# Optimization experiments

Measured on AMD Instinct MI355X. Metric: run time of the kernel, lower is better.

Reference implementation:

```python
import jax, jax.numpy as jnp
import numpy as np

N, E, B = 10000, 160000, 256
IN, DESC = 57, 1217
# (in_dim, heads, out_per_head) for the 4 GATConv layers
CONV_DIMS = [(57, 5, 114), (570, 5, 171), (855, 5, 114), (570, 1, 570)]
FC_DIMS = [(1024 + DESC, 1024), (1024, 2048), (2048, 1024), (1024, 256), (256, 1)]


def setup_inputs() -> dict:
    key = jax.random.key(0)
    cnt = [0]
    def p(shape, scale=0.05):
        cnt[0] += 1
        return jax.random.normal(jax.random.fold_in(key, cnt[0]), shape, jnp.float32) * scale
    d = {}
    d["x"] = jax.random.normal(jax.random.fold_in(key, 100), (N, IN), jnp.float32)
    d["edge_index"] = jax.random.randint(jax.random.fold_in(key, 101), (2, E), 0, N)
    d["batch"] = jnp.sort(jax.random.randint(jax.random.fold_in(key, 102), (N,), 0, B))
    d["desc"] = jax.random.normal(jax.random.fold_in(key, 103), (B, DESC), jnp.float32)
    for i, (ci, H, C) in enumerate(CONV_DIMS, 1):
        d[f"W{i}"] = p((ci, H * C))
        d[f"as{i}"] = p((H, C))
        d[f"ad{i}"] = p((H, C))
        d[f"b{i}"] = jnp.zeros((H * C,), jnp.float32)
    d["Wg"] = p((570, 1024)); d["bg"] = jnp.zeros((1024,), jnp.float32)
    for i, (ci, co) in enumerate(FC_DIMS, 1):
        d[f"Wf{i}"] = p((ci, co))
        d[f"bf{i}"] = jnp.zeros((co,), jnp.float32)
    return d


def gat_conv(x, src, dst, W, a_src, a_dst, b):
    """PyG GATConv (eval mode: attention dropout off), self-loops already in src/dst."""
    n = x.shape[0]
    H, C = a_src.shape
    h = (x @ W).reshape(n, H, C)                      # [N,H,C]
    al_s = (h * a_src).sum(-1)                         # [N,H]
    al_d = (h * a_dst).sum(-1)                         # [N,H]
    e = jax.nn.leaky_relu(al_s[src] + al_d[dst], 0.2)  # [E,H]
    # segment softmax over destination node
    m = jax.ops.segment_max(e, dst, num_segments=n)
    e = jnp.exp(e - m[dst])
    s = jax.ops.segment_sum(e, dst, num_segments=n)
    alpha = e / (s[dst] + 1e-16)                       # [E,H]
    msg = h[src] * alpha[:, :, None]                   # [E,H,C]
    out = jax.ops.segment_sum(msg, dst, num_segments=n)
    return out.reshape(n, H * C) + b


def reference(x, edge_index, batch, desc,
              W1, as1, ad1, b1, W2, as2, ad2, b2,
              W3, as3, ad3, b3, W4, as4, ad4, b4,
              Wg, bg, Wf1, bf1, Wf2, bf2, Wf3, bf3, Wf4, bf4, Wf5, bf5):
    n = x.shape[0]
    loops = jnp.arange(n)
    src = jnp.concatenate([edge_index[0], loops])
    dst = jnp.concatenate([edge_index[1], loops])
    h = x
    for W, a_s, a_d, b in [(W1, as1, ad1, b1), (W2, as2, ad2, b2),
                           (W3, as3, ad3, b3), (W4, as4, ad4, b4)]:
        h = jax.nn.relu(gat_conv(h, src, dst, W, a_s, a_d, b))
    pooled = jax.ops.segment_sum(h, batch, num_segments=B)   # global_add_pool [B,570]
    g = pooled @ Wg + bg
    z = jnp.concatenate([g, desc], axis=1)                    # [B, 2241]
    z = jax.nn.relu(z @ Wf1 + bf1)
    z = jax.nn.relu(z @ Wf2 + bf2)
    z = jax.nn.relu(z @ Wf3 + bf3)
    z = jax.nn.relu(z @ Wf4 + bf4)
    return z @ Wf5 + bf5                                      # [B,1]
```

## Files before the change

kernel.cpp:

```cpp
#include <hip/hip_runtime.h>
#include <hip/hip_bf16.h>
#include <math.h>

#define NNODES 10000
#define NEDGES 160000
#define NB     256
#define ETOT   (NEDGES + NNODES)
#define INDIM  57
#define DESCD  1217

static inline size_t align256(size_t x) { return (x + 255) & ~size_t(255); }

typedef _Float16 half8_t __attribute__((ext_vector_type(8)));
typedef _Float16 half4v_t __attribute__((ext_vector_type(4)));
typedef _Float16 half2_t __attribute__((ext_vector_type(2)));
typedef float f32x4 __attribute__((ext_vector_type(4)));

__device__ inline float wave_max(float v) {
#pragma unroll
  for (int o = 32; o > 0; o >>= 1) v = fmaxf(v, __shfl_xor(v, o));
  return v;
}
__device__ inline float wave_sum(float v) {
#pragma unroll
  for (int o = 32; o > 0; o >>= 1) v += __shfl_xor(v, o);
  return v;
}

__global__ void count_kernel(const int* __restrict__ ei, int* __restrict__ deg) {
  int e = blockIdx.x * blockDim.x + threadIdx.x;
  if (e < ETOT) {
    int dst = (e < NEDGES) ? ei[NEDGES + e] : (e - NEDGES);
    atomicAdd(&deg[dst], 1);
  }
}

__global__ __launch_bounds__(1024) void scan_kernel(const int* __restrict__ deg,
                                                    int* __restrict__ row_ptr,
                                                    int* __restrict__ cursor) {
  __shared__ int part[1024];
  const int CHUNK = (NNODES + 1023) / 1024;
  int t = threadIdx.x;
  int start = t * CHUNK;
  int sum = 0;
  for (int i = 0; i < CHUNK; ++i) {
    int idx = start + i;
    if (idx < NNODES) sum += deg[idx];
  }
  part[t] = sum;
  __syncthreads();
  for (int off = 1; off < 1024; off <<= 1) {
    int v = (t >= off) ? part[t - off] : 0;
    __syncthreads();
    part[t] += v;
    __syncthreads();
  }
  int run = (t > 0) ? part[t - 1] : 0;
  for (int i = 0; i < CHUNK; ++i) {
    int idx = start + i;
    if (idx < NNODES) {
      row_ptr[idx] = run;
      cursor[idx] = run;
      run += deg[idx];
    }
  }
  if (t == 1023) row_ptr[NNODES] = ETOT;
}

__global__ void scatter_kernel(const int* __restrict__ ei, int* __restrict__ cursor,
                               int* __restrict__ csr_src) {
  int e = blockIdx.x * blockDim.x + threadIdx.x;
  if (e < ETOT) {
    int src, dst;
    if (e < NEDGES) { src = ei[e]; dst = ei[NEDGES + e]; }
    else            { src = e - NEDGES; dst = src; }
    int idx = atomicAdd(&cursor[dst], 1);
    csr_src[idx] = src;
  }
}

__global__ void convert_x_kernel(const float* __restrict__ x, _Float16* __restrict__ x16) {
  int t = blockIdx.x * blockDim.x + threadIdx.x;
  if (t >= NNODES * 64) return;
  int n = t >> 6, k = t & 63;
  x16[t] = (_Float16)((k < INDIM) ? x[n * INDIM + k] : 0.f);
}

struct TMat { const float* src; _Float16* dst; int K, N, Kpad, tiles_k, tile_base;
              int Cn, Cnp, Ck, Ckp; };
struct TParams { TMat m[9]; };

__global__ __launch_bounds__(256) void transpose_w_kernel(TParams P, int nm) {
  __shared__ float tile[64][65];
  int bt = blockIdx.x;
  int mi = 0;
#pragma unroll
  for (int i = 1; i < 9; ++i)
    if (i < nm && bt >= P.m[i].tile_base) mi = i;
  TMat m = P.m[mi];
  int lt = bt - m.tile_base;
  int tk = lt % m.tiles_k, tn = lt / m.tiles_k;
  int k0 = tk * 64, n0 = tn * 64;
  int c = threadIdx.x & 63, r4 = threadIdx.x >> 6;
#pragma unroll
  for (int i = 0; i < 16; ++i) {
    int kr = r4 + i * 4;
    int gk = k0 + kr, gn = n0 + c;
    tile[kr][c] = (gk < m.K && gn < m.N) ? m.src[(size_t)gk * m.N + gn] : 0.f;
  }
  __syncthreads();
#pragma unroll
  for (int i = 0; i < 16; ++i) {
    int nr = r4 + i * 4;
    int gn = n0 + nr, gk = k0 + c;
    if (gn < m.N && gk < m.K) {
      int np = gn + (gn / m.Cn) * (m.Cnp - m.Cn);
      int kp = gk + (gk / m.Ck) * (m.Ckp - m.Ck);
      m.dst[(size_t)np * m.Kpad + kp] = (_Float16)tile[c][nr];
    }
  }
}

struct LMat { const float* W; const float* as; const float* ad; _Float16* dst;
              int K, HC, C, H, Kpad, la, wave_base, Ck, Ckp; };

__global__ __launch_bounds__(256) void logitw_kernel(LMat m0, LMat m1, LMat m2, LMat m3,
                                                     int nwaves) {
  int gw = (blockIdx.x * 256 + threadIdx.x) >> 6;
  int lane = threadIdx.x & 63;
  if (gw >= nwaves) return;
  LMat m = m3;
  if (gw < m1.wave_base) m = m0;
  else if (gw < m2.wave_base) m = m1;
  else if (gw < m3.wave_base) m = m2;
  int li = gw - m.wave_base;
  int H2 = 2 * m.H;
  int k = li / H2, r = li - k * H2;
  int h = (r >= m.H) ? r - m.H : r;
  const float* a = (r >= m.H) ? m.ad : m.as;
  float s = 0.f;
  for (int c = lane; c < m.C; c += 64)
    s += m.W[(size_t)k * m.HC + h * m.C + c] * a[h * m.C + c];
  s = wave_sum(s);
  int kp = k + (k / m.Ck) * (m.Ckp - m.Ck);
  if (lane == 0) m.dst[(size_t)(m.la + r) * m.Kpad + kp] = (_Float16)s;
}

__global__ void pooled16_kernel(const float* __restrict__ pooled, _Float16* __restrict__ p16) {
  int t = blockIdx.x * blockDim.x + threadIdx.x;
  if (t >= NB * 576) return;
  int b = t / 576, c = t - b * 576;
  p16[t] = (_Float16)((c < 570) ? pooled[b * 570 + c] : 0.f);
}

__global__ void desc_fill_kernel(const float* __restrict__ desc, _Float16* __restrict__ z16) {
  int t = blockIdx.x * blockDim.x + threadIdx.x;
  if (t >= NB * 1280) return;
  int b = t / 1280, i = t - b * 1280;
  z16[(size_t)b * 2304 + 1024 + i] = (_Float16)((i < DESCD) ? desc[b * DESCD + i] : 0.f);
}

__global__ __launch_bounds__(256) void mfma_gemm_kernel(
    const _Float16* __restrict__ A, const _Float16* __restrict__ Bt,
    _Float16* __restrict__ C, int M, int Kpad, int Nreal, int ldc) {
  __shared__ __align__(16) char smem[32768];
  char* AsB = smem;
  char* BsB = smem + 16384;
  int tid = threadIdx.x;
  int lane = tid & 63, wid = tid >> 6;
  int l15 = lane & 15, g = lane >> 4;
  int wr = wid >> 1, wc = wid & 1;
  int m0 = blockIdx.y * 128, n0 = blockIdx.x * 128;
  f32x4 acc[4][4];
#pragma unroll
  for (int i = 0; i < 4; ++i)
#pragma unroll
    for (int j = 0; j < 4; ++j) acc[i][j] = (f32x4){0.f, 0.f, 0.f, 0.f};

  int KT = Kpad >> 6;
  half8_t pa[4], pb[4];
#pragma unroll
  for (int i = 0; i < 4; ++i) {
    int r = i * 32 + (tid >> 3);
    int cs = (tid & 7) ^ (r & 7);
    int ga = min(m0 + r, M - 1);
    pa[i] = *(const half8_t*)(A + (size_t)ga * Kpad + cs * 8);
    pb[i] = *(const half8_t*)(Bt + (size_t)(n0 + r) * Kpad + cs * 8);
  }
  for (int kt = 0; kt < KT; ++kt) {
    __syncthreads();
#pragma unroll
    for (int i = 0; i < 4; ++i) {
      *(half8_t*)(AsB + i * 4096 + tid * 16) = pa[i];
      *(half8_t*)(BsB + i * 4096 + tid * 16) = pb[i];
    }
    __syncthreads();
    if (kt + 1 < KT) {
      int k0 = (kt + 1) << 6;
#pragma unroll
      for (int i = 0; i < 4; ++i) {
        int r = i * 32 + (tid >> 3);
        int cs = (tid & 7) ^ (r & 7);
        int ga = min(m0 + r, M - 1);
        pa[i] = *(const half8_t*)(A + (size_t)ga * Kpad + k0 + cs * 8);
        pb[i] = *(const half8_t*)(Bt + (size_t)(n0 + r) * Kpad + k0 + cs * 8);
      }
    }
#pragma unroll
    for (int kk = 0; kk < 2; ++kk) {
      half8_t af[4], bf[4];
#pragma unroll
      for (int f = 0; f < 4; ++f) {
        int ra = wr * 64 + f * 16 + l15;
        af[f] = *(const half8_t*)(AsB + ra * 128 + (((kk * 4 + g) ^ (ra & 7)) << 4));
        int cb = wc * 64 + f * 16 + l15;
        bf[f] = *(const half8_t*)(BsB + cb * 128 + (((kk * 4 + g) ^ (cb & 7)) << 4));
      }
#pragma unroll
      for (int fm = 0; fm < 4; ++fm)
#pragma unroll
        for (int fn = 0; fn < 4; ++fn)
          acc[fm][fn] = __builtin_amdgcn_mfma_f32_16x16x32_f16(af[fm], bf[fn], acc[fm][fn], 0, 0, 0);
    }
  }
#pragma unroll
  for (int fm = 0; fm < 4; ++fm) {
    int gmb = m0 + wr * 64 + fm * 16 + g * 4;
#pragma unroll
    for (int fn = 0; fn < 4; ++fn) {
      int gn = n0 + wc * 64 + fn * 16 + l15;
      if (gn >= Nreal) continue;
#pragma unroll
      for (int j = 0; j < 4; ++j) {
        int gm = gmb + j;
        if (gm < M) C[(size_t)gm * ldc + gn] = (_Float16)acc[fm][fn][j];
      }
    }
  }
}

__global__ __launch_bounds__(256) void mfma_splitk_kernel(
    const _Float16* __restrict__ A, const _Float16* __restrict__ Bt,
    float* __restrict__ P, int M, int Kpad, int N, int ktpc) {
  __shared__ __align__(16) char smem[32768];
  char* AsB = smem;
  char* BsB = smem + 16384;
  int tid = threadIdx.x;
  int lane = tid & 63, wid = tid >> 6;
  int l15 = lane & 15, g = lane >> 4;
  int wr = wid >> 1, wc = wid & 1;
  int m0 = blockIdx.y * 128, n0 = blockIdx.x * 128;
  int z = blockIdx.z;
  int KT = Kpad >> 6;
  int ktb = z * ktpc;
  int kte = min(KT, ktb + ktpc);
  f32x4 acc[4][4];
#pragma unroll
  for (int i = 0; i < 4; ++i)
#pragma unroll
    for (int j = 0; j < 4; ++j) acc[i][j] = (f32x4){0.f, 0.f, 0.f, 0.f};

  half8_t pa[4], pb[4];
  {
    int k0 = ktb << 6;
#pragma unroll
    for (int i = 0; i < 4; ++i) {
      int r = i * 32 + (tid >> 3);
      int cs = (tid & 7) ^ (r & 7);
      int ga = min(m0 + r, M - 1);
      pa[i] = *(const half8_t*)(A + (size_t)ga * Kpad + k0 + cs * 8);
      pb[i] = *(const half8_t*)(Bt + (size_t)(n0 + r) * Kpad + k0 + cs * 8);
    }
  }
  for (int kt = ktb; kt < kte; ++kt) {
    __syncthreads();
#pragma unroll
    for (int i = 0; i < 4; ++i) {
      *(half8_t*)(AsB + i * 4096 + tid * 16) = pa[i];
      *(half8_t*)(BsB + i * 4096 + tid * 16) = pb[i];
    }
    __syncthreads();
    if (kt + 1 < kte) {
      int k0 = (kt + 1) << 6;
#pragma unroll
      for (int i = 0; i < 4; ++i) {
        int r = i * 32 + (tid >> 3);
        int cs = (tid & 7) ^ (r & 7);
        int ga = min(m0 + r, M - 1);
        pa[i] = *(const half8_t*)(A + (size_t)ga * Kpad + k0 + cs * 8);
        pb[i] = *(const half8_t*)(Bt + (size_t)(n0 + r) * Kpad + k0 + cs * 8);
      }
    }
#pragma unroll
    for (int kk = 0; kk < 2; ++kk) {
      half8_t af[4], bf[4];
#pragma unroll
      for (int f = 0; f < 4; ++f) {
        int ra = wr * 64 + f * 16 + l15;
        af[f] = *(const half8_t*)(AsB + ra * 128 + (((kk * 4 + g) ^ (ra & 7)) << 4));
        int cb = wc * 64 + f * 16 + l15;
        bf[f] = *(const half8_t*)(BsB + cb * 128 + (((kk * 4 + g) ^ (cb & 7)) << 4));
      }
#pragma unroll
      for (int fm = 0; fm < 4; ++fm)
#pragma unroll
        for (int fn = 0; fn < 4; ++fn)
          acc[fm][fn] = __builtin_amdgcn_mfma_f32_16x16x32_f16(af[fm], bf[fn], acc[fm][fn], 0, 0, 0);
    }
  }
  size_t zb = (size_t)z * M;
#pragma unroll
  for (int fm = 0; fm < 4; ++fm) {
    int gmb = m0 + wr * 64 + fm * 16 + g * 4;
#pragma unroll
    for (int fn = 0; fn < 4; ++fn) {
      int gn = n0 + wc * 64 + fn * 16 + l15;
      if (gn >= N) continue;
#pragma unroll
      for (int j = 0; j < 4; ++j) {
        int gm = gmb + j;
        if (gm < M) P[(zb + gm) * N + gn] = acc[fm][fn][j];
      }
    }
  }
}

__global__ void reduce16_kernel(const float* __restrict__ P, const float* __restrict__ bias,
                                _Float16* __restrict__ O, int M, int N, int ldo,
                                int S, int relu) {
  int idx = blockIdx.x * blockDim.x + threadIdx.x;
  if (idx >= M * ldo) return;
  int row = idx / ldo, col = idx - row * ldo;
  if (col >= N) return;
  float s = bias[col];
  int MN = M * N;
  for (int z = 0; z < S; ++z) s += P[(size_t)z * MN + row * N + col];
  if (relu) s = fmaxf(s, 0.f);
  O[idx] = (_Float16)s;
}

__global__ __launch_bounds__(256) void fc5_kernel(const _Float16* __restrict__ A,
                                                  const float* __restrict__ w,
                                                  const float* __restrict__ b,
                                                  float* __restrict__ out) {
  int wid = threadIdx.x >> 6, lane = threadIdx.x & 63;
  int m = blockIdx.x * 4 + wid;
  if (m >= NB) return;
  float s = 0.f;
  for (int k = lane; k < 256; k += 64) s += (float)A[m * 256 + k] * w[k];
  s = wave_sum(s);
  if (lane == 0) out[m] = s + b[0];
}

template <int H>
__global__ __launch_bounds__(256) void att_kernel_t(const _Float16* __restrict__ hbuf,
                                                    int ldh, int la,
                                                    const int* __restrict__ row_ptr,
                                                    const int* __restrict__ csr_src,
                                                    _Float16* __restrict__ alpha_t,
                                                    half8_t* __restrict__ e8,
                                                    float* __restrict__ sinv) {
  int wid = threadIdx.x >> 6, lane = threadIdx.x & 63;
  int n = blockIdx.x * 4 + wid;
  if (n >= NNODES) return;
  int rp = row_ptr[n], deg = row_ptr[n + 1] - rp;
  float ad[H], m[H], ssum[H];
#pragma unroll
  for (int h = 0; h < H; ++h) {
    ad[h] = (float)hbuf[(size_t)n * ldh + la + H + h];
    m[h] = -1e30f; ssum[h] = 0.f;
  }
  for (int j = lane; j < deg; j += 64) {
    int s = csr_src[rp + j];
    half8_t v = *(const half8_t*)(hbuf + (size_t)s * ldh + la);
    half8_t ev{};
#pragma unroll
    for (int h = 0; h < H; ++h) {
      float e = (float)v[h] + ad[h];
      e = (e >= 0.f) ? e : 0.2f * e;
      ev[h] = (_Float16)e;
      m[h] = fmaxf(m[h], e);
    }
    e8[rp + j] = ev;
  }
#pragma unroll
  for (int h = 0; h < H; ++h) m[h] = wave_max(fmaxf(m[h], -1e30f));
  for (int j = lane; j < deg; j += 64) {
    half8_t ev = e8[rp + j];
#pragma unroll
    for (int h = 0; h < H; ++h) {
      float e = (float)ev[h] - m[h];
      e = (e > 0.f) ? 0.f : e;
      float x = expf(e);
      ssum[h] += x;
      alpha_t[(size_t)h * ETOT + rp + j] = (_Float16)x;
    }
  }
#pragma unroll
  for (int h = 0; h < H; ++h) {
    float s = wave_sum(ssum[h]);
    if (lane == 0) sinv[h * NNODES + n] = 1.f / (s + 1e-16f);
  }
}

__global__ __launch_bounds__(256) void agg_kernel(const _Float16* __restrict__ hbuf,
                                                  const _Float16* __restrict__ alpha_t,
                                                  const int* __restrict__ row_ptr,
                                                  const int* __restrict__ csr_src,
                                                  const float* __restrict__ bias,
                                                  const float* __restrict__ sinv,
                                                  _Float16* __restrict__ h16o,
                                                  int C, int Cpad, int ldh, int ldo,
                                                  int HCpad, int nchunks) {
  int wid = threadIdx.x >> 6, lane = threadIdx.x & 63;
  int gw = blockIdx.x * 4 + wid;
  int n = gw / nchunks, chunk = gw - n * nchunks;
  if (n >= NNODES) return;
  int k0 = chunk * 512 + lane * 8;
  if (k0 >= ldo) return;
  _Float16* op = h16o + (size_t)n * ldo + k0;
  if (k0 >= HCpad) { *(half8_t*)op = (half8_t){}; return; }
  int h0 = k0 / Cpad;
  int off = k0 - h0 * Cpad;
  const _Float16* A0 = alpha_t + (size_t)h0 * ETOT;
  const _Float16* hb = hbuf + k0;
  int rp = row_ptr[n], re = row_ptr[n + 1];
  half2_t acc0{}, acc1{}, acc2{}, acc3{};
  auto step = [&](int s, _Float16 a) {
    half8_t v = *(const half8_t*)(hb + (size_t)s * ldh);
    half2_t av{a, a};
    acc0 += av * half2_t{v[0], v[1]};
    acc1 += av * half2_t{v[2], v[3]};
    acc2 += av * half2_t{v[4], v[5]};
    acc3 += av * half2_t{v[6], v[7]};
  };
  int j = rp;
  for (; j < re && (j & 3); ++j) step(csr_src[j], A0[j]);
  for (; j + 8 <= re; j += 8) {
    int4 sa = *(const int4*)(csr_src + j);
    int4 sb = *(const int4*)(csr_src + j + 4);
    half4v_t aa = *(const half4v_t*)(A0 + j);
    half4v_t ab = *(const half4v_t*)(A0 + j + 4);
    step(sa.x, aa[0]); step(sa.y, aa[1]); step(sa.z, aa[2]); step(sa.w, aa[3]);
    step(sb.x, ab[0]); step(sb.y, ab[1]); step(sb.z, ab[2]); step(sb.w, ab[3]);
  }
  for (; j + 4 <= re; j += 4) {
    int4 sa = *(const int4*)(csr_src + j);
    half4v_t aa = *(const half4v_t*)(A0 + j);
    step(sa.x, aa[0]); step(sa.y, aa[1]); step(sa.z, aa[2]); step(sa.w, aa[3]);
  }
  for (; j < re; ++j) step(csr_src[j], A0[j]);
  float sc = sinv[h0 * NNODES + n];
  int base = h0 * C + off;
  int nreal = C - off;
  float af[8] = {(float)acc0[0], (float)acc0[1], (float)acc1[0], (float)acc1[1],
                 (float)acc2[0], (float)acc2[1], (float)acc3[0], (float)acc3[1]};
  half8_t o;
#pragma unroll
  for (int i = 0; i < 8; ++i) {
    float bv = bias[base + ((i < nreal) ? i : 0)];
    o[i] = (i < nreal) ? (_Float16)fmaxf(af[i] * sc + bv, 0.f) : (_Float16)0.f;
  }
  *(half8_t*)op = o;
}

__global__ __launch_bounds__(256) void pool_kernel(const _Float16* __restrict__ h4,
                                                   const int* __restrict__ batch,
                                                   float* __restrict__ pooled, int F, int ldh) {
  int wid = threadIdx.x >> 6, lane = threadIdx.x & 63;
  int n = blockIdx.x * 4 + wid;
  if (n >= NNODES) return;
  int b = batch[n];
  for (int k = lane; k < F; k += 64)
    atomicAdd(&pooled[(size_t)b * F + k], (float)h4[(size_t)n * ldh + k]);
}

extern "C" void kernel_launch(void* const* d_in, const int* in_sizes, int n_in,
                              void* d_out, int out_size, void* d_ws, size_t ws_size,
                              hipStream_t stream) {
  const float* x    = (const float*)d_in[0];
  const int*   ei   = (const int*)d_in[1];
  const int*   batch= (const int*)d_in[2];
  const float* desc = (const float*)d_in[3];
  const float* W1 = (const float*)d_in[4];  const float* as1 = (const float*)d_in[5];
  const float* ad1 = (const float*)d_in[6]; const float* b1 = (const float*)d_in[7];
  const float* W2 = (const float*)d_in[8];  const float* as2 = (const float*)d_in[9];
  const float* ad2 = (const float*)d_in[10];const float* b2 = (const float*)d_in[11];
  const float* W3 = (const float*)d_in[12]; const float* as3 = (const float*)d_in[13];
  const float* ad3 = (const float*)d_in[14];const float* b3 = (const float*)d_in[15];
  const float* W4 = (const float*)d_in[16]; const float* as4 = (const float*)d_in[17];
  const float* ad4 = (const float*)d_in[18];const float* b4 = (const float*)d_in[19];
  const float* Wg = (const float*)d_in[20]; const float* bg = (const float*)d_in[21];
  const float* Wf1 = (const float*)d_in[22];const float* bf1 = (const float*)d_in[23];
  const float* Wf2 = (const float*)d_in[24];const float* bf2 = (const float*)d_in[25];
  const float* Wf3 = (const float*)d_in[26];const float* bf3 = (const float*)d_in[27];
  const float* Wf4 = (const float*)d_in[28];const float* bf4 = (const float*)d_in[29];
  const float* Wf5 = (const float*)d_in[30];const float* bf5 = (const float*)d_in[31];
  float* out = (float*)d_out;

  char* p = (char*)d_ws;
  size_t off = 0;
  auto alloc = [&](size_t bytes) -> char* {
    char* r = p + off;
    off = align256(off + bytes);
    return r;
  };
  int*      deg     = (int*)alloc(sizeof(int) * NNODES);
  int*      row_ptr = (int*)alloc(sizeof(int) * (NNODES + 1));
  int*      cursor  = (int*)alloc(sizeof(int) * NNODES);
  int*      csr_src = (int*)alloc(sizeof(int) * ETOT);
  _Float16* alpha_t = (_Float16*)alloc(sizeof(_Float16) * (size_t)5 * ETOT);
  half8_t*  e8      = (half8_t*)alloc(sizeof(half8_t) * (size_t)ETOT);
  float*    sinv    = (float*)alloc(sizeof(float) * 5 * NNODES);
  _Float16* x16     = (_Float16*)alloc(sizeof(_Float16) * (size_t)NNODES * 64);
  _Float16* hA16    = (_Float16*)alloc(sizeof(_Float16) * ((size_t)NNODES * 896 + 1024));
  _Float16* h16     = (_Float16*)alloc(sizeof(_Float16) * ((size_t)NNODES * 896 + 1024));
  size_t wt_begin = off;
  _Float16* WtL1 = (_Float16*)alloc(sizeof(_Float16) * 640 * 64);
  _Float16* WtL2 = (_Float16*)alloc(sizeof(_Float16) * 896 * 640);
  _Float16* WtL3 = (_Float16*)alloc(sizeof(_Float16) * 640 * 896);
  _Float16* WtL4 = (_Float16*)alloc(sizeof(_Float16) * 640 * 640);
  _Float16* WtG  = (_Float16*)alloc(sizeof(_Float16) * 1024 * 576);
  _Float16* WtF1 = (_Float16*)alloc(sizeof(_Float16) * 1024 * 2304);
  _Float16* WtF2 = (_Float16*)alloc(sizeof(_Float16) * 2048 * 1024);
  _Float16* WtF3 = (_Float16*)alloc(sizeof(_Float16) * 1024 * 2048);
  _Float16* WtF4 = (_Float16*)alloc(sizeof(_Float16) * 256 * 1024);
  size_t wt_end = off;
  float*    pooled  = (float*)alloc(sizeof(float) * NB * 570);
  _Float16* p16     = (_Float16*)alloc(sizeof(_Float16) * NB * 576);
  _Float16* z16     = (_Float16*)alloc(sizeof(_Float16) * NB * 2304);
  _Float16* t16     = (_Float16*)alloc(sizeof(_Float16) * NB * 2048);
  _Float16* u16     = (_Float16*)alloc(sizeof(_Float16) * NB * 2048);
  _Float16* v16     = (_Float16*)alloc(sizeof(_Float16) * NB * 256);
  (void)ws_size;

  hipMemsetAsync(deg, 0, sizeof(int) * NNODES, stream);
  {
    dim3 g((ETOT + 255) / 256);
    count_kernel<<<g, 256, 0, stream>>>(ei, deg);
    scan_kernel<<<1, 1024, 0, stream>>>(deg, row_ptr, cursor);
    scatter_kernel<<<g, 256, 0, stream>>>(ei, cursor, csr_src);
  }
  convert_x_kernel<<<(NNODES * 64 + 255) / 256, 256, 0, stream>>>(x, x16);

  hipMemsetAsync(p + wt_begin, 0, wt_end - wt_begin, stream);
  {
    auto tiles = [](int K, int N) { return ((K + 63) / 64) * ((N + 63) / 64); };
    TParams tp;
    int base = 0;
    auto add = [&](int i, const float* src, _Float16* dst, int K, int N, int Kpad,
                   int Cn, int Cnp, int Ck, int Ckp) {
      tp.m[i] = { src, dst, K, N, Kpad, (K + 63) / 64, base, Cn, Cnp, Ck, Ckp };
      base += tiles(K, N);
    };
    add(0, W1,  WtL1, INDIM,        570,   64, 114, 120, INDIM, INDIM);
    add(1, W2,  WtL2, 570,          855,  640, 171, 176, 114, 120);
    add(2, W3,  WtL3, 855,          570,  896, 114, 120, 171, 176);
    add(3, W4,  WtL4, 570,          570,  640, 570, 570, 114, 120);
    add(4, Wg,  WtG,  570,          1024,  576, 1024, 1024, 570, 570);
    add(5, Wf1, WtF1, 1024 + DESCD, 1024, 2304, 1024, 1024, 2304, 2304);
    add(6, Wf2, WtF2, 1024,         2048, 1024, 2048, 2048, 1024, 1024);
    add(7, Wf3, WtF3, 2048,         1024, 2048, 1024, 1024, 2048, 2048);
    add(8, Wf4, WtF4, 1024,          256, 1024, 256, 256, 1024, 1024);
    transpose_w_kernel<<<base, 256, 0, stream>>>(tp, 9);
  }
  {
    LMat m0 = { W1, as1, ad1, WtL1, INDIM, 570, 114, 5,  64, 600, 0, INDIM, INDIM };
    LMat m1 = { W2, as2, ad2, WtL2, 570,   855, 171, 5, 640, 880, INDIM * 10, 114, 120 };
    LMat m2 = { W3, as3, ad3, WtL3, 855,   570, 114, 5, 896, 600, INDIM * 10 + 5700, 171, 176 };
    LMat m3 = { W4, as4, ad4, WtL4, 570,   570, 570, 1, 640, 576, INDIM * 10 + 5700 + 8550, 114, 120 };
    int nwaves = INDIM * 10 + 5700 + 8550 + 1140;
    logitw_kernel<<<(nwaves * 64 + 255) / 256, 256, 0, stream>>>(m0, m1, m2, m3, nwaves);
  }

  dim3 gnode((NNODES + 3) / 4);

  struct LayerDef { _Float16* Wt; const float* b;
                    int H, C, Cpad, HCpad, Kpad, Npad, ldh, la, Nreal, ldo; };
  LayerDef L[4] = {
    { WtL1, b1, 5, 114, 120, 600,  64, 640, 616, 600, 610, 640 },
    { WtL2, b2, 5, 171, 176, 880, 640, 896, 896, 880, 890, 896 },
    { WtL3, b3, 5, 114, 120, 600, 896, 640, 616, 600, 610, 640 },
    { WtL4, b4, 1, 570, 576, 576, 640, 640, 584, 576, 578, 576 },
  };
  for (int l = 0; l < 4; ++l) {
    {
      const _Float16* Ain = (l == 0) ? x16 : h16;
      dim3 g(L[l].Npad / 128, (NNODES + 127) / 128);
      mfma_gemm_kernel<<<g, 256, 0, stream>>>(Ain, L[l].Wt, hA16, NNODES, L[l].Kpad,
                                              L[l].Nreal, L[l].ldh);
    }
    if (L[l].H == 5)
      att_kernel_t<5><<<gnode, 256, 0, stream>>>(hA16, L[l].ldh, L[l].la,
                                                 row_ptr, csr_src, alpha_t, e8, sinv);
    else
      att_kernel_t<1><<<gnode, 256, 0, stream>>>(hA16, L[l].ldh, L[l].la,
                                                 row_ptr, csr_src, alpha_t, e8, sinv);
    {
      int nchunks = (L[l].ldo + 511) / 512;
      dim3 g((NNODES * nchunks + 3) / 4);
      agg_kernel<<<g, 256, 0, stream>>>(hA16, alpha_t, row_ptr, csr_src, L[l].b, sinv, h16,
                                        L[l].C, L[l].Cpad, L[l].ldh, L[l].ldo,
                                        L[l].HCpad, nchunks);
    }
  }

  hipMemsetAsync(pooled, 0, sizeof(float) * NB * 570, stream);
  pool_kernel<<<gnode, 256, 0, stream>>>(h16, batch, pooled, 570, 576);

  float* partials = (float*)hA16;
  auto head_gemm = [&](const _Float16* A, const _Float16* Wt, const float* bias,
                       _Float16* O, int Kpad, int N, int ldo, int relu,
                       int ktpc, int S) {
    dim3 g(N / 128, NB / 128, S);
    mfma_splitk_kernel<<<g, 256, 0, stream>>>(A, Wt, partials, NB, Kpad, N, ktpc);
    int totO = NB * ldo;
    reduce16_kernel<<<(totO + 255) / 256, 256, 0, stream>>>(partials, bias, O, NB, N, ldo, S, relu);
  };

  pooled16_kernel<<<(NB * 576 + 255) / 256, 256, 0, stream>>>(pooled, p16);
  head_gemm(p16, WtG, bg, z16, 576, 1024, 2304, 0, 3, 3);
  desc_fill_kernel<<<(NB * 1280 + 255) / 256, 256, 0, stream>>>(desc, z16);
  head_gemm(z16, WtF1, bf1, t16, 2304, 1024, 1024, 1, 3, 12);
  head_gemm(t16, WtF2, bf2, u16, 1024, 2048, 2048, 1, 2, 8);
  head_gemm(u16, WtF3, bf3, t16, 2048, 1024, 1024, 1, 2, 16);
  head_gemm(t16, WtF4, bf4, v16, 1024,  256,  256, 1, 1, 16);
  fc5_kernel<<<(NB + 3) / 4, 256, 0, stream>>>(v16, Wf5, bf5, out);
}
```

Baseline: 467.2 us.

## Replace split-K head GEMMs with 64x64-tile GEMM and fused bias/ReLU epilogue

The MLP head GEMMs move from 128x128 tiles with split-K partials plus a separate reduce kernel to 64x64 output tiles that run the full K loop and apply bias and ReLU in the epilogue. This drops one kernel launch per layer and the fp32 partial round trip through global memory. In exchange each block now walks all of K alone, so the per-block serial chain is longer and the grid is smaller for some layers (e.g. 16 blocks for the 256-wide layer). The M-boundary clamps are removed on the assumption that NB is a multiple of 64.

```diff
diff --git a/kernel.cpp b/kernel.cpp
--- a/kernel.cpp
+++ b/kernel.cpp
@@ -239,104 +239,85 @@
   }
 }
 
-__global__ __launch_bounds__(256) void mfma_splitk_kernel(
+__global__ __launch_bounds__(256) void mfma_gemm64_kernel(
     const _Float16* __restrict__ A, const _Float16* __restrict__ Bt,
-    float* __restrict__ P, int M, int Kpad, int N, int ktpc) {
-  __shared__ __align__(16) char smem[32768];
+    const float* __restrict__ bias, _Float16* __restrict__ O,
+    int Kpad, int ldc, int relu) {
+  __shared__ __align__(16) char smem[16384];
   char* AsB = smem;
-  char* BsB = smem + 16384;
+  char* BsB = smem + 8192;
   int tid = threadIdx.x;
   int lane = tid & 63, wid = tid >> 6;
   int l15 = lane & 15, g = lane >> 4;
   int wr = wid >> 1, wc = wid & 1;
-  int m0 = blockIdx.y * 128, n0 = blockIdx.x * 128;
-  int z = blockIdx.z;
+  int m0 = blockIdx.y * 64, n0 = blockIdx.x * 64;
+  f32x4 acc[2][2];
+#pragma unroll
+  for (int i = 0; i < 2; ++i)
+#pragma unroll
+    for (int j = 0; j < 2; ++j) acc[i][j] = (f32x4){0.f, 0.f, 0.f, 0.f};
+
   int KT = Kpad >> 6;
-  int ktb = z * ktpc;
-  int kte = min(KT, ktb + ktpc);
-  f32x4 acc[4][4];
-#pragma unroll
-  for (int i = 0; i < 4; ++i)
-#pragma unroll
-    for (int j = 0; j < 4; ++j) acc[i][j] = (f32x4){0.f, 0.f, 0.f, 0.f};
-
-  half8_t pa[4], pb[4];
-  {
-    int k0 = ktb << 6;
-#pragma unroll
-    for (int i = 0; i < 4; ++i) {
-      int r = i * 32 + (tid >> 3);
-      int cs = (tid & 7) ^ (r & 7);
-      int ga = min(m0 + r, M - 1);
-      pa[i] = *(const half8_t*)(A + (size_t)ga * Kpad + k0 + cs * 8);
-      pb[i] = *(const half8_t*)(Bt + (size_t)(n0 + r) * Kpad + k0 + cs * 8);
-    }
-  }
-  for (int kt = ktb; kt < kte; ++kt) {
+  int r = tid >> 2;
+  half8_t pa[2], pb[2];
+#pragma unroll
+  for (int i = 0; i < 2; ++i) {
+    int cc = (tid & 3) + 4 * i;
+    int cs = cc ^ (r & 7);
+    pa[i] = *(const half8_t*)(A + (size_t)(m0 + r) * Kpad + cs * 8);
+    pb[i] = *(const half8_t*)(Bt + (size_t)(n0 + r) * Kpad + cs * 8);
+  }
+  for (int kt = 0; kt < KT; ++kt) {
     __syncthreads();
 #pragma unroll
-    for (int i = 0; i < 4; ++i) {
-      *(half8_t*)(AsB + i * 4096 + tid * 16) = pa[i];
-      *(half8_t*)(BsB + i * 4096 + tid * 16) = pb[i];
+    for (int i = 0; i < 2; ++i) {
+      int cc = (tid & 3) + 4 * i;
+      *(half8_t*)(AsB + r * 128 + cc * 16) = pa[i];
+      *(half8_t*)(BsB + r * 128 + cc * 16) = pb[i];
     }
     __syncthreads();
-    if (kt + 1 < kte) {
+    if (kt + 1 < KT) {
       int k0 = (kt + 1) << 6;
 #pragma unroll
-      for (int i = 0; i < 4; ++i) {
-        int r = i * 32 + (tid >> 3);
-        int cs = (tid & 7) ^ (r & 7);
-        int ga = min(m0 + r, M - 1);
-        pa[i] = *(const half8_t*)(A + (size_t)ga * Kpad + k0 + cs * 8);
+      for (int i = 0; i < 2; ++i) {
+        int cc = (tid & 3) + 4 * i;
+        int cs = cc ^ (r & 7);
+        pa[i] = *(const half8_t*)(A + (size_t)(m0 + r) * Kpad + k0 + cs * 8);
         pb[i] = *(const half8_t*)(Bt + (size_t)(n0 + r) * Kpad + k0 + cs * 8);
       }
     }
 #pragma unroll
     for (int kk = 0; kk < 2; ++kk) {
-      half8_t af[4], bf[4];
-#pragma unroll
-      for (int f = 0; f < 4; ++f) {
-        int ra = wr * 64 + f * 16 + l15;
+      half8_t af[2], bf[2];
+#pragma unroll
+      for (int f = 0; f < 2; ++f) {
+        int ra = wr * 32 + f * 16 + l15;
         af[f] = *(const half8_t*)(AsB + ra * 128 + (((kk * 4 + g) ^ (ra & 7)) << 4));
-        int cb = wc * 64 + f * 16 + l15;
+        int cb = wc * 32 + f * 16 + l15;
         bf[f] = *(const half8_t*)(BsB + cb * 128 + (((kk * 4 + g) ^ (cb & 7)) << 4));
       }
 #pragma unroll
-      for (int fm = 0; fm < 4; ++fm)
-#pragma unroll
-        for (int fn = 0; fn < 4; ++fn)
+      for (int fm = 0; fm < 2; ++fm)
+#pragma unroll
+        for (int fn = 0; fn < 2; ++fn)
           acc[fm][fn] = __builtin_amdgcn_mfma_f32_16x16x32_f16(af[fm], bf[fn], acc[fm][fn], 0, 0, 0);
     }
   }
-  size_t zb = (size_t)z * M;
-#pragma unroll
-  for (int fm = 0; fm < 4; ++fm) {
-    int gmb = m0 + wr * 64 + fm * 16 + g * 4;
-#pragma unroll
-    for (int fn = 0; fn < 4; ++fn) {
-      int gn = n0 + wc * 64 + fn * 16 + l15;
-      if (gn >= N) continue;
+#pragma unroll
+  for (int fm = 0; fm < 2; ++fm) {
+    int gmb = m0 + wr * 32 + fm * 16 + g * 4;
+#pragma unroll
+    for (int fn = 0; fn < 2; ++fn) {
+      int gn = n0 + wc * 32 + fn * 16 + l15;
+      float bv = bias[gn];
 #pragma unroll
       for (int j = 0; j < 4; ++j) {
-        int gm = gmb + j;
-        if (gm < M) P[(zb + gm) * N + gn] = acc[fm][fn][j];
+        float v = acc[fm][fn][j] + bv;
+        if (relu) v = fmaxf(v, 0.f);
+        O[(size_t)(gmb + j) * ldc + gn] = (_Float16)v;
       }
     }
   }
-}
-
-__global__ void reduce16_kernel(const float* __restrict__ P, const float* __restrict__ bias,
-                                _Float16* __restrict__ O, int M, int N, int ldo,
-                                int S, int relu) {
-  int idx = blockIdx.x * blockDim.x + threadIdx.x;
-  if (idx >= M * ldo) return;
-  int row = idx / ldo, col = idx - row * ldo;
-  if (col >= N) return;
-  float s = bias[col];
-  int MN = M * N;
-  for (int z = 0; z < S; ++z) s += P[(size_t)z * MN + row * N + col];
-  if (relu) s = fmaxf(s, 0.f);
-  O[idx] = (_Float16)s;
 }
 
 __global__ __launch_bounds__(256) void fc5_kernel(const _Float16* __restrict__ A,
@@ -608,22 +589,18 @@
   hipMemsetAsync(pooled, 0, sizeof(float) * NB * 570, stream);
   pool_kernel<<<gnode, 256, 0, stream>>>(h16, batch, pooled, 570, 576);
 
-  float* partials = (float*)hA16;
   auto head_gemm = [&](const _Float16* A, const _Float16* Wt, const float* bias,
-                       _Float16* O, int Kpad, int N, int ldo, int relu,
-                       int ktpc, int S) {
-    dim3 g(N / 128, NB / 128, S);
-    mfma_splitk_kernel<<<g, 256, 0, stream>>>(A, Wt, partials, NB, Kpad, N, ktpc);
-    int totO = NB * ldo;
-    reduce16_kernel<<<(totO + 255) / 256, 256, 0, stream>>>(partials, bias, O, NB, N, ldo, S, relu);
+                       _Float16* O, int Kpad, int N, int ldc, int relu) {
+    dim3 g(N / 64, NB / 64);
+    mfma_gemm64_kernel<<<g, 256, 0, stream>>>(A, Wt, bias, O, Kpad, ldc, relu);
   };
 
   pooled16_kernel<<<(NB * 576 + 255) / 256, 256, 0, stream>>>(pooled, p16);
-  head_gemm(p16, WtG, bg, z16, 576, 1024, 2304, 0, 3, 3);
+  head_gemm(p16, WtG, bg, z16, 576, 1024, 2304, 0);
   desc_fill_kernel<<<(NB * 1280 + 255) / 256, 256, 0, stream>>>(desc, z16);
-  head_gemm(z16, WtF1, bf1, t16, 2304, 1024, 1024, 1, 3, 12);
-  head_gemm(t16, WtF2, bf2, u16, 1024, 2048, 2048, 1, 2, 8);
-  head_gemm(u16, WtF3, bf3, t16, 2048, 1024, 1024, 1, 2, 16);
-  head_gemm(t16, WtF4, bf4, v16, 1024,  256,  256, 1, 1, 16);
+  head_gemm(z16, WtF1, bf1, t16, 2304, 1024, 1024, 1);
+  head_gemm(t16, WtF2, bf2, u16, 1024, 2048, 2048, 1);
+  head_gemm(u16, WtF3, bf3, t16, 2048, 1024, 1024, 1);
+  head_gemm(t16, WtF4, bf4, v16, 1024,  256,  256, 1);
   fc5_kernel<<<(NB + 3) / 4, 256, 0, stream>>>(v16, Wf5, bf5, out);
 }
```

Measured after the change: 463.5 us. No clear change (-0.8%).
